# Kernel optimization log

Hardware: AMD Instinct MI355X
Metric: run time of the kernel (lower is better)

## Reference

```python
import jax, jax.numpy as jnp
import numpy as np

TOP_K = 2  # cfg.num_experts_per_tok
INIT_STD = 0.02


def setup_inputs() -> dict:
    key = jax.random.key(0)
    ks = jax.random.split(key, 6)
    B, S, D, F, E = 4, 2048, 1024, 4096, 8
    return {
        "residual": jax.random.normal(ks[0], (B, S, D), dtype=jnp.float32),
        "W_router": jax.random.normal(ks[1], (E, D), dtype=jnp.float32) * INIT_STD,
        "W_in": jax.random.normal(ks[2], (E, D, F), dtype=jnp.float32) * INIT_STD,
        "b_in": jnp.zeros((E, F), dtype=jnp.float32),
        "W_out": jax.random.normal(ks[3], (E, F, D), dtype=jnp.float32) * INIT_STD,
        "b_out": jnp.zeros((E, D), dtype=jnp.float32),
    }


def reference(residual, W_router, W_in, b_in, W_out, b_out):
    B, S, D = residual.shape
    E = W_router.shape[0]
    x = residual.reshape(-1, D)                      # [T, D], T = B*S

    # Router: softmax over experts, pick top-k, renormalize selected weights.
    logits = jnp.einsum('td,ed->te', x, W_router)    # [T, E]
    probs = jax.nn.softmax(logits, axis=-1)
    top_w, top_i = jax.lax.top_k(probs, TOP_K)       # [T, K]
    top_w = top_w / jnp.sum(top_w, axis=-1, keepdims=True)

    # Dense combine weights [T, E]; zero for non-selected experts.
    combine = jnp.sum(jax.nn.one_hot(top_i, E, dtype=x.dtype) * top_w[..., None], axis=1)

    # Weighted sum of expert MLP outputs (GELU experts, exact erf as in torch).
    y = jnp.zeros_like(x)
    for e in range(E):  # small fixed expert count
        h = jax.nn.gelu(x @ W_in[e] + b_in[e], approximate=False)   # [T, F]
        y = y + combine[:, e:e + 1] * (h @ W_out[e] + b_out[e])     # [T, D]
    return y.reshape(B, S, D)
```

## Files before the change

### kernel.cpp

```cpp
#include <hip/hip_runtime.h>
#include <hip/hip_bf16.h>
#include <math.h>

#define T_TOK 8192
#define DMODEL 1024
#define FFN 4096
#define NEXP 8
#define NSLOT (T_TOK * 2)
#define MAXT 136

typedef _Float16 f16;
typedef _Float16 half8 __attribute__((ext_vector_type(8)));
typedef _Float16 half4 __attribute__((ext_vector_type(4)));
typedef float f32x4 __attribute__((ext_vector_type(4)));
typedef unsigned int u32;

__device__ __forceinline__ void gll16(const void* g, void* l) {
  __builtin_amdgcn_global_load_lds(
      (const __attribute__((address_space(1))) u32*)g,
      (__attribute__((address_space(3))) u32*)l, 16, 0, 0);
}

__device__ __forceinline__ float gelu_fast(float v) {
  float x = fabsf(v) * 0.70710678118654752f;
  float t = 1.0f / (1.0f + 0.3275911f * x);
  float poly = ((((1.061405429f * t - 1.453152027f) * t + 1.421413741f) * t -
                 0.284496736f) * t + 0.254829592f) * t;
  float erf_ = 1.0f - poly * __expf(-x * x);
  erf_ = copysignf(erf_, v);
  return 0.5f * v * (1.0f + erf_);
}

__device__ __forceinline__ float gelu_exact(float v) {
  return 0.5f * v * (1.0f + erff(v * 0.70710678118654752f));
}

__device__ __forceinline__ void transq_tile(const float* __restrict__ ip,
                                            f16* __restrict__ op, int R, int C,
                                            int r0, int c0, char* smemraw) {
  float* tile = (float*)smemraw;
  int tid = threadIdx.x;
  int q = tid & 15;
  int rr = tid >> 4;
#pragma unroll
  for (int p = 0; p < 8; p++) {
    int row = rr + p * 16;
    float4 v = *(const float4*)(ip + (size_t)(r0 + row) * C + c0 + q * 4);
    int qs = (q + (row >> 3)) & 15;
    *(float4*)(tile + row * 64 + qs * 4) = v;
  }
  __syncthreads();
#pragma unroll
  for (int p = 0; p < 4; p++) {
    int idx = tid + p * 256;
    int c = idx >> 4;
    int b = idx & 15;
    half8 h;
#pragma unroll
    for (int i = 0; i < 8; i++) {
      int row = b * 8 + i;
      int qs = (((c >> 2) + b) & 15);
      h[i] = (f16)tile[row * 64 + qs * 4 + (c & 3)];
    }
    *(half8*)(op + (size_t)(c0 + c) * R + r0 + b * 8) = h;
  }
}

__global__ __launch_bounds__(256) void prepA_k(
    const float* __restrict__ x, const float* __restrict__ Wr,
    const float* __restrict__ Wi,
    int* __restrict__ sel_e, float* __restrict__ sel_w,
    f16* __restrict__ xh, f16* __restrict__ WiT) {
  __shared__ __align__(16) char smem[32768];
  if (blockIdx.x < 4096) {
    int e = blockIdx.x >> 9;
    int idx = blockIdx.x & 511;
    int rt = idx >> 6, ct = idx & 63;
    transq_tile(Wi + (size_t)e * DMODEL * FFN, WiT + (size_t)e * DMODEL * FFN,
                DMODEL, FFN, rt * 128, ct * 64, smem);
  } else {
    int rb = blockIdx.x - 4096;
    int t = rb * 4 + (threadIdx.x >> 6);
    int lane = threadIdx.x & 63;
    const float* xp = x + (size_t)t * DMODEL;
    f16* xhp = xh + (size_t)t * DMODEL;
    float p[NEXP];
#pragma unroll
    for (int e = 0; e < NEXP; e++) p[e] = 0.f;
#pragma unroll
    for (int q = 0; q < 4; q++) {
      float4 xv = *(const float4*)(xp + q * 256 + lane * 4);
      half4 h;
      h[0] = (f16)xv.x; h[1] = (f16)xv.y; h[2] = (f16)xv.z; h[3] = (f16)xv.w;
      *(half4*)(xhp + q * 256 + lane * 4) = h;
#pragma unroll
      for (int e = 0; e < NEXP; e++) {
        float4 wv = *(const float4*)(Wr + e * DMODEL + q * 256 + lane * 4);
        p[e] += xv.x * wv.x + xv.y * wv.y + xv.z * wv.z + xv.w * wv.w;
      }
    }
#pragma unroll
    for (int off = 32; off; off >>= 1) {
#pragma unroll
      for (int e = 0; e < NEXP; e++) p[e] += __shfl_xor(p[e], off);
    }
    if (lane == 0) {
      float l0 = -1e30f, l1 = -1e30f;
      int e0 = 0, e1 = 1;
#pragma unroll
      for (int e = 0; e < NEXP; e++) {
        if (p[e] > l0) { l1 = l0; e1 = e0; l0 = p[e]; e0 = e; }
        else if (p[e] > l1) { l1 = p[e]; e1 = e; }
      }
      float r = expf(l1 - l0);
      float inv = 1.f / (1.f + r);
      sel_e[t * 2] = e0;     sel_w[t * 2] = inv;
      sel_e[t * 2 + 1] = e1; sel_w[t * 2 + 1] = r * inv;
    }
  }
}

__global__ __launch_bounds__(256) void count_sched_k(
    const int* __restrict__ sel_e, int* __restrict__ meta) {
  __shared__ int cnts[NEXP];
  int tid = threadIdx.x;
  if (tid < NEXP) cnts[tid] = 0;
  __syncthreads();
  int c0 = 0, c1 = 0, c2 = 0, c3 = 0, c4 = 0, c5 = 0, c6 = 0, c7 = 0;
  for (int i = tid; i < NSLOT; i += 256) {
    int v = sel_e[i];
    c0 += (v == 0); c1 += (v == 1); c2 += (v == 2); c3 += (v == 3);
    c4 += (v == 4); c5 += (v == 5); c6 += (v == 6); c7 += (v == 7);
  }
#pragma unroll
  for (int off = 32; off; off >>= 1) {
    c0 += __shfl_down(c0, off); c1 += __shfl_down(c1, off);
    c2 += __shfl_down(c2, off); c3 += __shfl_down(c3, off);
    c4 += __shfl_down(c4, off); c5 += __shfl_down(c5, off);
    c6 += __shfl_down(c6, off); c7 += __shfl_down(c7, off);
  }
  if ((tid & 63) == 0) {
    atomicAdd(&cnts[0], c0); atomicAdd(&cnts[1], c1);
    atomicAdd(&cnts[2], c2); atomicAdd(&cnts[3], c3);
    atomicAdd(&cnts[4], c4); atomicAdd(&cnts[5], c5);
    atomicAdd(&cnts[6], c6); atomicAdd(&cnts[7], c7);
  }
  __syncthreads();
  if (tid == 0) {
    int* counts = meta;
    int* fill = meta + 64;
    int* offs = meta + 128;
    int* tE = meta + 256;
    int* tR0 = meta + 512;
    int* tRows = meta + 768;
    int off = 0, nt = 0;
    for (int e = 0; e < NEXP; e++) {
      counts[e] = cnts[e];
      offs[e] = off;
      fill[e] = 0;
      int c = cnts[e];
      for (int t0 = 0; t0 < c; t0 += 128) {
        tE[nt] = e; tR0[nt] = off + t0; tRows[nt] = min(128, c - t0); nt++;
      }
      off += c;
    }
    offs[NEXP] = off;
    for (; nt < MAXT; nt++) tE[nt] = -1;
  }
}

__global__ __launch_bounds__(256) void scatter_k(
    const int* __restrict__ sel_e, const float* __restrict__ sel_w,
    const int* __restrict__ offs, int* fill,
    int* __restrict__ row_tok, float* __restrict__ row_w) {
  int s = blockIdx.x * 256 + threadIdx.x;
  int e = sel_e[s];
  int pos = atomicAdd(&fill[e], 1);
  int r = offs[e] + pos;
  row_tok[r] = s >> 1;
  row_w[r] = sel_w[s];
}

__global__ __launch_bounds__(256, 4) void gemm1_k(
    const f16* __restrict__ Xh, const f16* __restrict__ Wt,
    const float* __restrict__ b_in, f16* __restrict__ H,
    const int* __restrict__ meta,
    const float* __restrict__ Wo, f16* __restrict__ WoT) {
  __shared__ __align__(16) char smem[33792];

  if (blockIdx.x >= MAXT * 32) {
    int bid = blockIdx.x - MAXT * 32;
    int e = bid >> 9;
    int idx = bid & 511;
    int rt = idx >> 4, ct = idx & 15;
    transq_tile(Wo + (size_t)e * DMODEL * FFN, WoT + (size_t)e * DMODEL * FFN,
                FFN, DMODEL, rt * 128, ct * 64, smem);
    return;
  }
  int bid2 = blockIdx.x;
  int xcd = bid2 & 7, bidx = bid2 >> 3;
  int wg = xcd * ((MAXT * 32) >> 3) + bidx;
  int tm = wg >> 5;
  int n0 = (wg & 31) * 128;
  int e = (meta + 256)[tm];
  if (e < 0) return;
  int row0 = (meta + 512)[tm];
  int nrows = (meta + 768)[tm];
  const int* row_tok = meta + 1024 + 2 * NSLOT;

  int tid = threadIdx.x, lane = tid & 63, wid = tid >> 6;
  int wrow = wid >> 1, wcol = wid & 1;
  int l15 = lane & 15, l4 = lane >> 4;

  u32 aoffs[4], boffs[4];
#pragma unroll
  for (int p = 0; p < 4; p++) {
    int L = tid + p * 256;
    int row = L >> 3, ch = L & 7;
    int cs = ch ^ (row & 7);
    aoffs[p] = (u32)(row_tok[min(row0 + row, NSLOT - 1)] * (DMODEL * 2) + cs * 16);
    boffs[p] = (u32)((e * FFN + n0 + row) * (DMODEL * 2) + cs * 16);
  }
  const char* gA = (const char*)Xh;
  const char* gB = (const char*)Wt;

  f32x4 acc[4][4];
#pragma unroll
  for (int m = 0; m < 4; m++)
#pragma unroll
    for (int n = 0; n < 4; n++) acc[m][n] = (f32x4)0.f;

  const int NT = DMODEL / 64;
  for (int kt = 0; kt < NT; ++kt) {
#pragma unroll
    for (int p = 0; p < 4; p++) {
      gll16(gA + aoffs[p], smem + (tid + p * 256) * 16);
      gll16(gB + boffs[p], smem + 16384 + (tid + p * 256) * 16);
      aoffs[p] += 128; boffs[p] += 128;
    }
    __syncthreads();
#pragma unroll
    for (int s = 0; s < 2; s++) {
      int swz = ((s * 4 + l4) ^ (l15 & 7)) << 4;
      const char* pA = smem + (wrow * 64 + l15) * 128 + swz;
      const char* pB = smem + 16384 + (wcol * 64 + l15) * 128 + swz;
      half8 a[4], b[4];
#pragma unroll
      for (int i = 0; i < 4; i++) a[i] = *(const half8*)(pA + i * 2048);
#pragma unroll
      for (int j = 0; j < 4; j++) b[j] = *(const half8*)(pB + j * 2048);
#pragma unroll
      for (int i = 0; i < 4; i++)
#pragma unroll
        for (int j = 0; j < 4; j++)
          acc[i][j] = __builtin_amdgcn_mfma_f32_16x16x32_f16(a[i], b[j], acc[i][j], 0, 0, 0);
    }
    __syncthreads();
  }

  float bias[4];
#pragma unroll
  for (int n = 0; n < 4; n++) bias[n] = b_in[e * FFN + n0 + wcol * 64 + n * 16 + l15];
#pragma unroll
  for (int m = 0; m < 4; m++)
#pragma unroll
    for (int n = 0; n < 4; n++)
#pragma unroll
      for (int j = 0; j < 4; j++) {
        int row = wrow * 64 + m * 16 + l4 * 4 + j;
        int col = wcol * 64 + n * 16 + l15;
        *(f16*)(smem + row * 264 + col * 2) = (f16)gelu_fast(acc[m][n][j] + bias[n]);
      }
  __syncthreads();
#pragma unroll
  for (int p = 0; p < 8; ++p) {
    int idx = tid + p * 256;
    int row = idx >> 4, cc = idx & 15;
    if (row < nrows) {
      f32x4 v = *(const f32x4*)(smem + row * 264 + cc * 16);
      __builtin_nontemporal_store(
          v, (f32x4*)(H + (size_t)(row0 + row) * FFN + n0 + cc * 8));
    }
  }
}

__global__ __launch_bounds__(256, 4) void gemm2_k(
    const f16* __restrict__ H, const f16* __restrict__ Wt,
    const float* __restrict__ b_out, float* __restrict__ out,
    const int* __restrict__ meta) {
  int xcd = blockIdx.x & 7, bidx = blockIdx.x >> 3;
  int wg = xcd * (gridDim.x >> 3) + bidx;
  int tm = wg >> 4;
  int r4 = wg & 15;
  int n0 = (r4 & 7) * 128;
  int ks = r4 >> 3;
  int e = (meta + 256)[tm];
  if (e < 0) return;
  int row0 = (meta + 512)[tm];
  int nrows = (meta + 768)[tm];
  const int* row_tok = meta + 1024 + 2 * NSLOT;
  const float* row_w = (const float*)(meta + 1024 + 3 * NSLOT);

  __shared__ __align__(16) char smem[32768];

  int tid = threadIdx.x, lane = tid & 63, wid = tid >> 6;
  int wrow = wid >> 1, wcol = wid & 1;
  int l15 = lane & 15, l4 = lane >> 4;
  u32 k0b = (u32)(ks * (FFN / 2) * 2);

  u32 aoffs[4], boffs[4];
#pragma unroll
  for (int p = 0; p < 4; p++) {
    int L = tid + p * 256;
    int row = L >> 3, ch = L & 7;
    int cs = ch ^ (row & 7);
    aoffs[p] = (u32)((u32)min(row0 + row, NSLOT - 1) * (FFN * 2) + k0b + cs * 16);
    boffs[p] = (u32)((u32)(e * DMODEL + n0 + row) * (FFN * 2) + k0b + cs * 16);
  }
  const char* gA = (const char*)H;
  const char* gB = (const char*)Wt;

  f32x4 acc[4][4];
#pragma unroll
  for (int m = 0; m < 4; m++)
#pragma unroll
    for (int n = 0; n < 4; n++) acc[m][n] = (f32x4)0.f;

  const int NT = (FFN / 2) / 64;
  for (int kt = 0; kt < NT; ++kt) {
#pragma unroll
    for (int p = 0; p < 4; p++) {
      gll16(gA + aoffs[p], smem + (tid + p * 256) * 16);
      gll16(gB + boffs[p], smem + 16384 + (tid + p * 256) * 16);
      aoffs[p] += 128; boffs[p] += 128;
    }
    __syncthreads();
#pragma unroll
    for (int s = 0; s < 2; s++) {
      int swz = ((s * 4 + l4) ^ (l15 & 7)) << 4;
      const char* pA = smem + (wrow * 64 + l15) * 128 + swz;
      const char* pB = smem + 16384 + (wcol * 64 + l15) * 128 + swz;
      half8 a[4], b[4];
#pragma unroll
      for (int i = 0; i < 4; i++) a[i] = *(const half8*)(pA + i * 2048);
#pragma unroll
      for (int j = 0; j < 4; j++) b[j] = *(const half8*)(pB + j * 2048);
#pragma unroll
      for (int i = 0; i < 4; i++)
#pragma unroll
        for (int j = 0; j < 4; j++)
          acc[i][j] = __builtin_amdgcn_mfma_f32_16x16x32_f16(a[i], b[j], acc[i][j], 0, 0, 0);
    }
    __syncthreads();
  }

  float bias[4];
#pragma unroll
  for (int n = 0; n < 4; n++)
    bias[n] = (ks == 0) ? b_out[e * DMODEL + n0 + wcol * 64 + n * 16 + l15] : 0.f;
#pragma unroll
  for (int m = 0; m < 4; m++)
#pragma unroll
    for (int j = 0; j < 4; j++) {
      int r = wrow * 64 + m * 16 + l4 * 4 + j;
      if (r < nrows) {
        int rg = row0 + r;
        int tok = row_tok[rg];
        float w = row_w[rg];
#pragma unroll
        for (int n = 0; n < 4; n++)
          atomicAdd(out + (size_t)tok * DMODEL + n0 + wcol * 64 + n * 16 + l15,
                    w * (acc[m][n][j] + bias[n]));
      }
    }
}

__global__ __launch_bounds__(256) void naive_k(
    const float* __restrict__ x, const float* __restrict__ W_in,
    const float* __restrict__ b_in, const float* __restrict__ W_out,
    const float* __restrict__ b_out, const int* __restrict__ sel_e,
    const float* __restrict__ sel_w, float* __restrict__ out) {
  int s = blockIdx.x;
  int t = s >> 1;
  int e = sel_e[s];
  float w = sel_w[s];
  __shared__ float xs[DMODEL];
  __shared__ float hs[FFN];
  int tid = threadIdx.x;
  for (int d = tid; d < DMODEL; d += 256) xs[d] = x[(size_t)t * DMODEL + d];
  __syncthreads();
  for (int f = tid; f < FFN; f += 256) {
    float a = b_in[e * FFN + f];
    const float* wp = W_in + (size_t)e * DMODEL * FFN + f;
    for (int d = 0; d < DMODEL; d++) a += xs[d] * wp[(size_t)d * FFN];
    hs[f] = gelu_exact(a);
  }
  __syncthreads();
  for (int d = tid; d < DMODEL; d += 256) {
    float a = b_out[e * DMODEL + d];
    const float* wp = W_out + (size_t)e * FFN * DMODEL + d;
    for (int f = 0; f < FFN; f++) a += hs[f] * wp[(size_t)f * DMODEL];
    atomicAdd(&out[(size_t)t * DMODEL + d], w * a);
  }
}

__global__ __launch_bounds__(256) void router_k(
    const float* __restrict__ x, const float* __restrict__ Wr,
    int* __restrict__ sel_e, float* __restrict__ sel_w) {
  int t = blockIdx.x * 4 + (threadIdx.x >> 6);
  int lane = threadIdx.x & 63;
  const float* xp = x + (size_t)t * DMODEL;
  float p[NEXP];
#pragma unroll
  for (int e = 0; e < NEXP; e++) p[e] = 0.f;
#pragma unroll
  for (int i = 0; i < DMODEL / 64; i++) {
    float xv = xp[lane + i * 64];
#pragma unroll
    for (int e = 0; e < NEXP; e++) p[e] += xv * Wr[e * DMODEL + lane + i * 64];
  }
#pragma unroll
  for (int off = 32; off; off >>= 1) {
#pragma unroll
    for (int e = 0; e < NEXP; e++) p[e] += __shfl_xor(p[e], off);
  }
  if (lane == 0) {
    float l0 = -1e30f, l1 = -1e30f;
    int e0 = 0, e1 = 1;
#pragma unroll
    for (int e = 0; e < NEXP; e++) {
      if (p[e] > l0) { l1 = l0; e1 = e0; l0 = p[e]; e0 = e; }
      else if (p[e] > l1) { l1 = p[e]; e1 = e; }
    }
    float r = expf(l1 - l0);
    float inv = 1.f / (1.f + r);
    sel_e[t * 2] = e0;     sel_w[t * 2] = inv;
    sel_e[t * 2 + 1] = e1; sel_w[t * 2 + 1] = r * inv;
  }
}

extern "C" void kernel_launch(void* const* d_in, const int* in_sizes, int n_in,
                              void* d_out, int out_size, void* d_ws, size_t ws_size,
                              hipStream_t stream) {
  const float* residual = (const float*)d_in[0];
  const float* W_router = (const float*)d_in[1];
  const float* W_in = (const float*)d_in[2];
  const float* b_in = (const float*)d_in[3];
  const float* W_out = (const float*)d_in[4];
  const float* b_out = (const float*)d_in[5];
  float* out = (float*)d_out;

  char* ws = (char*)d_ws;
  int* meta = (int*)ws;
  size_t off = (size_t)1 << 20;
  f16* Xh = (f16*)(ws + off); off += (size_t)T_TOK * DMODEL * 2;
  f16* Wih = (f16*)(ws + off); off += (size_t)NEXP * DMODEL * FFN * 2;
  f16* Woh = (f16*)(ws + off); off += (size_t)NEXP * DMODEL * FFN * 2;
  f16* H = (f16*)(ws + off); off += (size_t)NSLOT * FFN * 2;
  off += 65536;
  bool fast = ws_size >= off;

  int* sel_e = meta + 1024;
  float* sel_w = (float*)(meta + 1024 + NSLOT);
  int* row_tok = meta + 1024 + 2 * NSLOT;
  float* row_w = (float*)(meta + 1024 + 3 * NSLOT);

  hipMemsetAsync(meta, 0, 4096, stream);
  hipMemsetAsync(d_out, 0, (size_t)out_size * sizeof(float), stream);

  if (fast) {
    prepA_k<<<4096 + T_TOK / 4, 256, 0, stream>>>(
        residual, W_router, W_in, sel_e, sel_w, Xh, Wih);
    count_sched_k<<<1, 256, 0, stream>>>(sel_e, meta);
    scatter_k<<<NSLOT / 256, 256, 0, stream>>>(sel_e, sel_w, meta + 128, meta + 64,
                                               row_tok, row_w);
    gemm1_k<<<MAXT * 32 + 4096, 256, 0, stream>>>(Xh, Wih, b_in, H, meta,
                                                  W_out, Woh);
    gemm2_k<<<MAXT * 16, 256, 0, stream>>>(H, Woh, b_out, out, meta);
  } else {
    router_k<<<T_TOK / 4, 256, 0, stream>>>(residual, W_router, sel_e, sel_w);
    naive_k<<<NSLOT, 256, 0, stream>>>(residual, W_in, b_in, W_out, b_out,
                                       sel_e, sel_w, out);
  }
}
```

Before: 560.7 us.

## Replace gemm2 atomic scatter-add with per-split f16 buffers and gather combine kernel

gemm2 no longer does fp32 atomicAdd into the output per token row. Each K-split now writes its bias-added f16 partial tile, sorted by expert row, into one of two buffers (reusing the W_in f16 workspace). A new combine kernel then uses an inverse slot map, built in scatter_k, to gather both experts' two partials per token, weight them and write fp32 output. This removes the output memset and the metadata memset. gemm1 and gemm2 also switch to a per-wave shared-memory epilogue without a block barrier, with launch bounds occupancy lowered from 4 to 3. The trade-off is an extra kernel launch, extra global traffic for the partial buffers, and f16 rounding of the partial sums.

```diff
diff --git a/kernel.cpp b/kernel.cpp
--- a/kernel.cpp
+++ b/kernel.cpp
@@ -172,21 +172,23 @@
 __global__ __launch_bounds__(256) void scatter_k(
     const int* __restrict__ sel_e, const float* __restrict__ sel_w,
     const int* __restrict__ offs, int* fill,
-    int* __restrict__ row_tok, float* __restrict__ row_w) {
+    int* __restrict__ row_tok, float* __restrict__ row_w,
+    int* __restrict__ inv) {
   int s = blockIdx.x * 256 + threadIdx.x;
   int e = sel_e[s];
   int pos = atomicAdd(&fill[e], 1);
   int r = offs[e] + pos;
   row_tok[r] = s >> 1;
   row_w[r] = sel_w[s];
-}
-
-__global__ __launch_bounds__(256, 4) void gemm1_k(
+  inv[s] = r;
+}
+
+__global__ __launch_bounds__(256, 3) void gemm1_k(
     const f16* __restrict__ Xh, const f16* __restrict__ Wt,
     const float* __restrict__ b_in, f16* __restrict__ H,
     const int* __restrict__ meta,
     const float* __restrict__ Wo, f16* __restrict__ WoT) {
-  __shared__ __align__(16) char smem[33792];
+  __shared__ __align__(16) char smem[36864];
 
   if (blockIdx.x >= MAXT * 32) {
     int bid = blockIdx.x - MAXT * 32;
@@ -258,6 +260,7 @@
     __syncthreads();
   }
 
+  char* wsm = smem + wid * 9216;
   float bias[4];
 #pragma unroll
   for (int n = 0; n < 4; n++) bias[n] = b_in[e * FFN + n0 + wcol * 64 + n * 16 + l15];
@@ -267,27 +270,26 @@
     for (int n = 0; n < 4; n++)
 #pragma unroll
       for (int j = 0; j < 4; j++) {
-        int row = wrow * 64 + m * 16 + l4 * 4 + j;
-        int col = wcol * 64 + n * 16 + l15;
-        *(f16*)(smem + row * 264 + col * 2) = (f16)gelu_fast(acc[m][n][j] + bias[n]);
+        int lrow = m * 16 + l4 * 4 + j;
+        *(f16*)(wsm + lrow * 144 + (n * 16 + l15) * 2) =
+            (f16)gelu_fast(acc[m][n][j] + bias[n]);
       }
-  __syncthreads();
 #pragma unroll
   for (int p = 0; p < 8; ++p) {
-    int idx = tid + p * 256;
-    int row = idx >> 4, cc = idx & 15;
-    if (row < nrows) {
-      f32x4 v = *(const f32x4*)(smem + row * 264 + cc * 16);
+    int lr = (lane >> 3) + p * 8;
+    if (wrow * 64 + lr < nrows) {
+      f32x4 v = *(const f32x4*)(wsm + lr * 144 + (lane & 7) * 16);
       __builtin_nontemporal_store(
-          v, (f32x4*)(H + (size_t)(row0 + row) * FFN + n0 + cc * 8));
-    }
-  }
-}
-
-__global__ __launch_bounds__(256, 4) void gemm2_k(
+          v, (f32x4*)(H + (size_t)(row0 + wrow * 64 + lr) * FFN + n0 +
+                      wcol * 64 + (lane & 7) * 8));
+    }
+  }
+}
+
+__global__ __launch_bounds__(256, 3) void gemm2_k(
     const f16* __restrict__ H, const f16* __restrict__ Wt,
-    const float* __restrict__ b_out, float* __restrict__ out,
-    const int* __restrict__ meta) {
+    const float* __restrict__ b_out, f16* __restrict__ Y0,
+    f16* __restrict__ Y1, const int* __restrict__ meta) {
   int xcd = blockIdx.x & 7, bidx = blockIdx.x >> 3;
   int wg = xcd * (gridDim.x >> 3) + bidx;
   int tm = wg >> 4;
@@ -298,10 +300,8 @@
   if (e < 0) return;
   int row0 = (meta + 512)[tm];
   int nrows = (meta + 768)[tm];
-  const int* row_tok = meta + 1024 + 2 * NSLOT;
-  const float* row_w = (const float*)(meta + 1024 + 3 * NSLOT);
-
-  __shared__ __align__(16) char smem[32768];
+
+  __shared__ __align__(16) char smem[36864];
 
   int tid = threadIdx.x, lane = tid & 63, wid = tid >> 6;
   int wrow = wid >> 1, wcol = wid & 1;
@@ -354,6 +354,8 @@
     __syncthreads();
   }
 
+  f16* Y = ks ? Y1 : Y0;
+  char* wsm = smem + wid * 9216;
   float bias[4];
 #pragma unroll
   for (int n = 0; n < 4; n++)
@@ -361,18 +363,52 @@
 #pragma unroll
   for (int m = 0; m < 4; m++)
 #pragma unroll
-    for (int j = 0; j < 4; j++) {
-      int r = wrow * 64 + m * 16 + l4 * 4 + j;
-      if (r < nrows) {
-        int rg = row0 + r;
-        int tok = row_tok[rg];
-        float w = row_w[rg];
-#pragma unroll
-        for (int n = 0; n < 4; n++)
-          atomicAdd(out + (size_t)tok * DMODEL + n0 + wcol * 64 + n * 16 + l15,
-                    w * (acc[m][n][j] + bias[n]));
+    for (int n = 0; n < 4; n++)
+#pragma unroll
+      for (int j = 0; j < 4; j++) {
+        int lrow = m * 16 + l4 * 4 + j;
+        *(f16*)(wsm + lrow * 144 + (n * 16 + l15) * 2) =
+            (f16)(acc[m][n][j] + bias[n]);
       }
-    }
+#pragma unroll
+  for (int p = 0; p < 8; ++p) {
+    int lr = (lane >> 3) + p * 8;
+    if (wrow * 64 + lr < nrows) {
+      f32x4 v = *(const f32x4*)(wsm + lr * 144 + (lane & 7) * 16);
+      __builtin_nontemporal_store(
+          v, (f32x4*)(Y + (size_t)(row0 + wrow * 64 + lr) * DMODEL + n0 +
+                      wcol * 64 + (lane & 7) * 8));
+    }
+  }
+}
+
+__global__ __launch_bounds__(256) void combine_k(
+    const f16* __restrict__ Y0, const f16* __restrict__ Y1,
+    const int* __restrict__ inv, const float* __restrict__ row_w,
+    float* __restrict__ out) {
+  int t = blockIdx.x * 4 + (threadIdx.x >> 6);
+  int lane = threadIdx.x & 63;
+  int r0 = inv[2 * t], r1 = inv[2 * t + 1];
+  float w0 = row_w[r0], w1 = row_w[r1];
+  int d0 = lane * 16;
+  const half8* a0 = (const half8*)(Y0 + (size_t)r0 * DMODEL + d0);
+  const half8* a1 = (const half8*)(Y1 + (size_t)r0 * DMODEL + d0);
+  const half8* b0 = (const half8*)(Y0 + (size_t)r1 * DMODEL + d0);
+  const half8* b1 = (const half8*)(Y1 + (size_t)r1 * DMODEL + d0);
+  float* op = out + (size_t)t * DMODEL + d0;
+#pragma unroll
+  for (int q = 0; q < 2; q++) {
+    half8 x0 = a0[q], x1 = a1[q], y0 = b0[q], y1 = b1[q];
+    float r[8];
+#pragma unroll
+    for (int i = 0; i < 8; i++)
+      r[i] = w0 * ((float)x0[i] + (float)x1[i]) +
+             w1 * ((float)y0[i] + (float)y1[i]);
+    f32x4 v1 = {r[0], r[1], r[2], r[3]};
+    f32x4 v2 = {r[4], r[5], r[6], r[7]};
+    *(f32x4*)(op + q * 8) = v1;
+    *(f32x4*)(op + q * 8 + 4) = v2;
+  }
 }
 
 __global__ __launch_bounds__(256) void naive_k(
@@ -460,24 +496,27 @@
   off += 65536;
   bool fast = ws_size >= off;
 
+  f16* Y0 = Wih;
+  f16* Y1 = Wih + (size_t)NSLOT * DMODEL;
+
   int* sel_e = meta + 1024;
   float* sel_w = (float*)(meta + 1024 + NSLOT);
   int* row_tok = meta + 1024 + 2 * NSLOT;
   float* row_w = (float*)(meta + 1024 + 3 * NSLOT);
-
-  hipMemsetAsync(meta, 0, 4096, stream);
-  hipMemsetAsync(d_out, 0, (size_t)out_size * sizeof(float), stream);
+  int* inv = meta + 1024 + 4 * NSLOT;
 
   if (fast) {
     prepA_k<<<4096 + T_TOK / 4, 256, 0, stream>>>(
         residual, W_router, W_in, sel_e, sel_w, Xh, Wih);
     count_sched_k<<<1, 256, 0, stream>>>(sel_e, meta);
     scatter_k<<<NSLOT / 256, 256, 0, stream>>>(sel_e, sel_w, meta + 128, meta + 64,
-                                               row_tok, row_w);
+                                               row_tok, row_w, inv);
     gemm1_k<<<MAXT * 32 + 4096, 256, 0, stream>>>(Xh, Wih, b_in, H, meta,
                                                   W_out, Woh);
-    gemm2_k<<<MAXT * 16, 256, 0, stream>>>(H, Woh, b_out, out, meta);
+    gemm2_k<<<MAXT * 16, 256, 0, stream>>>(H, Woh, b_out, Y0, Y1, meta);
+    combine_k<<<T_TOK / 4, 256, 0, stream>>>(Y0, Y1, inv, row_w, out);
   } else {
+    hipMemsetAsync(d_out, 0, (size_t)out_size * sizeof(float), stream);
     router_k<<<T_TOK / 4, 256, 0, stream>>>(residual, W_router, sel_e, sel_w);
     naive_k<<<NSLOT, 256, 0, stream>>>(residual, W_in, b_in, W_out, b_out,
                                        sel_e, sel_w, out);
```

After: 520.0 us. -7.3%, faster.
